# Optimization experiments

Hardware: AMD Instinct MI355X
Metric: run time of the kernel (lower is better)

## Reference

```python
import jax, jax.numpy as jnp
import numpy as np

T = 32          # n_node_types
EXTRA = 3       # input_dim = T + 3
D = 9           # perfect binary tree depth -> N = 2**D - 1 = 511 nodes/plan
N = 2 ** D - 1
EMB = 64
HID = 64
FC = 64
OUT = 8         # N_METRICS
NS = 5          # N_SAMPLES
P = 2560        # number of plans (P // NS = 512 groups)
B = 512


def setup_inputs() -> dict:
    key = jax.random.key(0)
    ks = jax.random.split(key, 8)

    def lin(k, o, i):
        return (jax.random.normal(k, (o, i), jnp.float32) / np.sqrt(i)).astype(jnp.float32)

    x0 = jax.random.normal(ks[0], (P, N, T + EXTRA), jnp.float32)
    x = jax.random.uniform(ks[1], (B, P // NS), jnp.float32)
    return {
        "x": x,
        "x0": x0,
        "W_emb": lin(ks[2], EMB, T), "b_emb": jnp.zeros((EMB,), jnp.float32),
        "W0": lin(ks[3], HID, EMB + EXTRA), "b0": jnp.zeros((HID,), jnp.float32),
        "W1": lin(ks[4], HID, EMB + EXTRA + 2 * HID), "b1": jnp.zeros((HID,), jnp.float32),
        "Wfc1": lin(ks[5], FC, HID), "bfc1": jnp.zeros((FC,), jnp.float32),
        "Wfc2": lin(ks[6], OUT, FC), "bfc2": jnp.zeros((OUT,), jnp.float32),
    }


def reference(x, x0, W_emb, b_emb, W0, b0, W1, b1, Wfc1, bfc1, Wfc2, bfc2):
    # --- enc_dnn: per-node embed + concat(extra, children hiddens) + Linear + ReLU ---
    # node_emb = emb(xi[:T]); node_input = [node_emb, xi[T:], h_children...]
    emb = jnp.einsum('pnt,et->pne', x0[..., :T], W_emb) + b_emb    # [P,N,EMB]
    feats = jnp.concatenate([emb, x0[..., T:]], axis=-1)           # [P,N,EMB+3]
    # heap layout: node i's children are 2i+1, 2i+2; level l occupies [2^l-1, 2^{l+1}-1)
    lo = 2 ** (D - 1) - 1
    h = jax.nn.relu(jnp.einsum('pnf,hf->pnh', feats[:, lo:], W0) + b0)  # leaves
    for l in range(D - 2, -1, -1):  # structural loop over tree levels (fixed, small)
        lo, n = 2 ** l - 1, 2 ** l
        f = feats[:, lo:lo + n]
        inp = jnp.concatenate([f, h[:, 0::2], h[:, 1::2]], axis=-1)  # [emb|extra|h_left|h_right]
        h = jax.nn.relu(jnp.einsum('pnf,hf->pnh', inp, W1) + b1)
    h0 = h[:, 0]                                                   # root hidden, [P,HID]
    # --- agg_weight ---
    mean_h = h0.reshape(-1, NS, HID).mean(axis=1)                  # [P/NS, HID]
    weighted = x @ mean_h                                          # [B, HID]
    hid = jax.nn.relu(weighted @ Wfc1.T + bfc1)
    return hid @ Wfc2.T + bfc2                                     # [B, OUT]
```

## Files before the change

### kernel.cpp

```cpp
#include <hip/hip_runtime.h>
#include <hip/hip_bf16.h>


typedef __attribute__((ext_vector_type(8))) short s8v;
typedef __attribute__((ext_vector_type(4))) float f4v;
typedef unsigned short u16;
typedef unsigned int   u32;

__device__ __forceinline__ u16 f2bf(float f) {
    return __builtin_bit_cast(u16, __float2bfloat16(f));
}
__device__ __forceinline__ f4v mfma16(s8v a, s8v b, f4v c) {
    return __builtin_amdgcn_mfma_f32_16x16x32_bf16(a, b, c, 0, 0, 0);
}
#define SWZ(r) ((((r) & 1) | (((r) >> 1) & 6)) << 3)

__device__ __forceinline__ u32 pk2(float a, float b) {
    return (u32)f2bf(fmaxf(a, 0.f)) | ((u32)f2bf(fmaxf(b, 0.f)) << 16);
}
__device__ __forceinline__ s8v pkfrag(f4v h0, f4v h1) {
    int4 d;
    d.x = (int)pk2(h0[0], h0[1]); d.y = (int)pk2(h0[2], h0[3]);
    d.z = (int)pk2(h1[0], h1[1]); d.w = (int)pk2(h1[2], h1[3]);
    return __builtin_bit_cast(s8v, d);
}
__device__ __forceinline__ s8v mkB0(float4 A, float4 B) {
    s8v r;
    r[0]=(short)f2bf(A.x); r[1]=(short)f2bf(A.y); r[2]=(short)f2bf(A.z); r[3]=(short)f2bf(A.w);
    r[4]=(short)f2bf(B.x); r[5]=(short)f2bf(B.y); r[6]=(short)f2bf(B.z); r[7]=(short)f2bf(B.w);
    return r;
}
__device__ __forceinline__ s8v mkB1(float4 T) {
    s8v r = (s8v){0,0,0,0,0,0,0,0};
    r[0]=(short)f2bf(T.y); r[1]=(short)f2bf(T.z); r[2]=(short)f2bf(T.w);
    return r;
}
__device__ __forceinline__ s8v xB0(const float* __restrict__ xr, int lq) {
    return mkB0(*(const float4*)(xr + lq * 8), *(const float4*)(xr + lq * 8 + 4));
}
__device__ __forceinline__ s8v xB1(const float* __restrict__ xr, int lq) {
    s8v r = (s8v){0,0,0,0,0,0,0,0};
    if (lq == 0) {
        float4 T = *(const float4*)(xr + 31);
        r[0]=(short)f2bf(T.y); r[1]=(short)f2bf(T.z); r[2]=(short)f2bf(T.w);
    }
    return r;
}
__device__ __forceinline__ s8v wread(const u16* w, int stride, int row, int ks, int lq) {
    return *(const s8v*)(w + row * stride + ks * 32 + lq * 8);
}
__device__ __forceinline__ f4v bias4(const float* __restrict__ b) {
    float4 t = *(const float4*)b; return (f4v){t.x, t.y, t.z, t.w};
}
__device__ __forceinline__ int sigp(int rho, int s, int h) {
    return 32*s + 4*h + ((rho & 12) << 1) + (rho & 3);
}

__global__ void prep_kernel(const float* __restrict__ W_emb, const float* __restrict__ b_emb,
                            const float* __restrict__ W0, const float* __restrict__ b0,
                            const float* __restrict__ W1, const float* __restrict__ b1,
                            u16* __restrict__ wt1, u16* __restrict__ wt0,
                            float* __restrict__ b1p, float* __restrict__ b0p)
{
    int idx = blockIdx.x * 256 + threadIdx.x;
    if (idx < 64 * 192) {
        int h = idx / 192, k = idx % 192;
        float v;
        if (k < 32) { v = 0.f; for (int e = 0; e < 64; e++) v = fmaf(W1[h*195+e], W_emb[e*32+k], v); }
        else if (k < 35)  v = W1[h*195 + 64 + (k - 32)];
        else if (k < 64)  v = 0.f;
        else              v = W1[h*195 + 67 + (k - 64)];
        wt1[h*192 + k] = f2bf(v);
    } else if (idx < 64*192 + 64*64) {
        int j = idx - 64*192; int h = j >> 6, k = j & 63;
        float v;
        if (k < 32)      { v = 0.f; for (int e = 0; e < 64; e++) v = fmaf(W0[h*67+e], W_emb[e*32+k], v); }
        else if (k < 35)   v = W0[h*67 + 64 + (k - 32)];
        else               v = 0.f;
        wt0[h*64 + k] = f2bf(v);
    } else if (idx < 64*192 + 64*64 + 64) {
        int h = idx - (64*192 + 64*64);
        float v = b1[h];
        for (int e = 0; e < 64; e++) v = fmaf(W1[h*195+e], b_emb[e], v);
        b1p[h] = v;
    } else if (idx < 64*192 + 64*64 + 128) {
        int h = idx - (64*192 + 64*64 + 64);
        float v = b0[h];
        for (int e = 0; e < 64; e++) v = fmaf(W0[h*67+e], b_emb[e], v);
        b0p[h] = v;
    }
}

__global__ __launch_bounds__(512, 2) void tree_all(
    const float* __restrict__ x0,
    const u16* __restrict__ wt1g, const u16* __restrict__ wt0g,
    const float* __restrict__ b1p, const float* __restrict__ b0p,
    float* __restrict__ h0out)
{
    __shared__ __align__(16) u16 wt1s[64 * 200];
    __shared__ __align__(16) u16 wt0s[64 * 40 + 64];
    __shared__ __align__(16) u16 buf6[4 * 64 * 64];

    const int tid = threadIdx.x;
    const int l   = tid & 63;
    const int w   = tid >> 6;
    const int lq  = l >> 4;
    const int rho = l & 15;
    const int pair = w >> 2;
    const int c    = w & 3;
    const int tA = blockIdx.x * 4 + 2 * pair;
    const int tB = tA + 1;
    const float* xbA = x0 + (size_t)tA * 511 * 35;
    const float* xbB = x0 + (size_t)tB * 511 * 35;

    const float* xq0A = xbA + (size_t)(255 + 64*c + 4*rho) * 35;
    const float* xq0B = xbB + (size_t)(255 + 64*c + 4*rho) * 35;
    float4 pAa = *(const float4*)(xq0A + lq*8);
    float4 pAb = *(const float4*)(xq0A + lq*8 + 4);
    float4 pAt = (lq == 0) ? *(const float4*)(xq0A + 31) : float4{0.f,0.f,0.f,0.f};
    float4 pBa = *(const float4*)(xq0B + lq*8);
    float4 pBb = *(const float4*)(xq0B + lq*8 + 4);
    float4 pBt = (lq == 0) ? *(const float4*)(xq0B + 31) : float4{0.f,0.f,0.f,0.f};

    {
        u32* d1 = (u32*)wt1s; const u32* s1 = (const u32*)wt1g;
        #pragma unroll
        for (int t = 0; t < 12; t++) {
            int i = t*512 + tid;
            int row = i / 96, kk = i - row*96;
            d1[row*100 + kk] = s1[row*96 + kk];
        }
        u32* d0 = (u32*)wt0s; const u32* s0 = (const u32*)wt0g;
        #pragma unroll
        for (int t = 0; t < 3; t++) {
            int i = t*512 + tid;
            if (i < 1280) { int row = i / 20, kk = i - row*20; d0[row*20 + kk] = s0[row*32 + kk]; }
        }
        if (tid < 32) ((u32*)(wt0s + 64*40))[tid] = 0;
    }
    __syncthreads();

    s8v TLA[4][2], TLB[4][2];
    {
        s8v WL[4][2]; f4v bL[4];
        #pragma unroll
        for (int i = 0; i < 4; i++) {
            int sg = sigp(rho, i >> 1, i & 1);
            WL[i][0] = wread(wt0s, 40, sg, 0, lq);
            WL[i][1] = wread(wt0s, 40, sg, 1, lq);
            bL[i] = bias4(b0p + 32*(i>>1) + 8*lq + 4*(i&1));
        }
        auto leafstep = [&](s8v xaA, s8v xtA, s8v xaB, s8v xtB, int q) {
            f4v aA[4], aB[4];
            #pragma unroll
            for (int i = 0; i < 4; i++) { aA[i] = bL[i]; aB[i] = bL[i]; }
            #pragma unroll
            for (int i = 0; i < 4; i++) {
                aA[i] = mfma16(WL[i][0], xaA, aA[i]);
                aA[i] = mfma16(WL[i][1], xtA, aA[i]);
                aB[i] = mfma16(WL[i][0], xaB, aB[i]);
                aB[i] = mfma16(WL[i][1], xtB, aB[i]);
            }
            TLA[q][0] = pkfrag(aA[0], aA[1]); TLA[q][1] = pkfrag(aA[2], aA[3]);
            TLB[q][0] = pkfrag(aB[0], aB[1]); TLB[q][1] = pkfrag(aB[2], aB[3]);
        };
        leafstep(mkB0(pAa, pAb), mkB1(pAt), mkB0(pBa, pBb), mkB1(pBt), 0);
        #pragma unroll
        for (int q = 1; q < 4; q++) {
            const float* xrA = xbA + (size_t)(255 + 64*c + 4*rho + q) * 35;
            const float* xrB = xbB + (size_t)(255 + 64*c + 4*rho + q) * 35;
            leafstep(xB0(xrA, lq), xB1(xrA, lq), xB0(xrB, lq), xB1(xrB, lq), q);
        }
    }

    s8v A7[4], B7[4];
    {
        f4v aAE[4], aAO[4], aBE[4], aBO[4];
        #pragma unroll
        for (int i = 0; i < 4; i++) {
            f4v b = bias4(b1p + 32*(i>>1) + 8*lq + 4*(i&1));
            aAE[i] = b; aAO[i] = b; aBE[i] = b; aBO[i] = b;
        }
        {
            const float* xrAE = xbA + (size_t)(127 + 32*c + 2*rho) * 35;
            const float* xrBE = xbB + (size_t)(127 + 32*c + 2*rho) * 35;
            s8v xAE0 = xB0(xrAE, lq),      xAE1 = xB1(xrAE, lq);
            s8v xAO0 = xB0(xrAE + 35, lq), xAO1 = xB1(xrAE + 35, lq);
            s8v xBE0 = xB0(xrBE, lq),      xBE1 = xB1(xrBE, lq);
            s8v xBO0 = xB0(xrBE + 35, lq), xBO1 = xB1(xrBE + 35, lq);
            #pragma unroll
            for (int i = 0; i < 4; i++) {
                int sg = sigp(rho, i >> 1, i & 1);
                s8v w0 = wread(wt1s, 200, sg, 0, lq);
                s8v w1 = wread(wt1s, 200, sg, 1, lq);
                aAE[i] = mfma16(w0, xAE0, aAE[i]); aAE[i] = mfma16(w1, xAE1, aAE[i]);
                aAO[i] = mfma16(w0, xAO0, aAO[i]); aAO[i] = mfma16(w1, xAO1, aAO[i]);
                aBE[i] = mfma16(w0, xBE0, aBE[i]); aBE[i] = mfma16(w1, xBE1, aBE[i]);
                aBO[i] = mfma16(w0, xBO0, aBO[i]); aBO[i] = mfma16(w1, xBO1, aBO[i]);
            }
        }
        #pragma unroll
        for (int i = 0; i < 4; i++) {
            int sg = sigp(rho, i >> 1, i & 1);
            s8v w2 = wread(wt1s, 200, sg, 2, lq);
            s8v w3 = wread(wt1s, 200, sg, 3, lq);
            s8v w4 = wread(wt1s, 200, sg, 4, lq);
            s8v w5 = wread(wt1s, 200, sg, 5, lq);
            aAE[i] = mfma16(w2, TLA[0][0], aAE[i]); aAE[i] = mfma16(w3, TLA[0][1], aAE[i]);
            aAE[i] = mfma16(w4, TLA[1][0], aAE[i]); aAE[i] = mfma16(w5, TLA[1][1], aAE[i]);
            aAO[i] = mfma16(w2, TLA[2][0], aAO[i]); aAO[i] = mfma16(w3, TLA[2][1], aAO[i]);
            aAO[i] = mfma16(w4, TLA[3][0], aAO[i]); aAO[i] = mfma16(w5, TLA[3][1], aAO[i]);
            aBE[i] = mfma16(w2, TLB[0][0], aBE[i]); aBE[i] = mfma16(w3, TLB[0][1], aBE[i]);
            aBE[i] = mfma16(w4, TLB[1][0], aBE[i]); aBE[i] = mfma16(w5, TLB[1][1], aBE[i]);
            aBO[i] = mfma16(w2, TLB[2][0], aBO[i]); aBO[i] = mfma16(w3, TLB[2][1], aBO[i]);
            aBO[i] = mfma16(w4, TLB[3][0], aBO[i]); aBO[i] = mfma16(w5, TLB[3][1], aBO[i]);
        }
        A7[0] = pkfrag(aAE[0], aAE[1]); A7[1] = pkfrag(aAE[2], aAE[3]);
        A7[2] = pkfrag(aAO[0], aAO[1]); A7[3] = pkfrag(aAO[2], aAO[3]);
        B7[0] = pkfrag(aBE[0], aBE[1]); B7[1] = pkfrag(aBE[2], aBE[3]);
        B7[2] = pkfrag(aBO[0], aBO[1]); B7[3] = pkfrag(aBO[2], aBO[3]);
    }

    {
        const float* xrA6 = xbA + (size_t)(63 + 16*c + rho) * 35;
        const float* xrB6 = xbB + (size_t)(63 + 16*c + rho) * 35;
        s8v xA0 = xB0(xrA6, lq), xA1 = xB1(xrA6, lq);
        s8v xBv0 = xB0(xrB6, lq), xBv1 = xB1(xrB6, lq);
        u16* slA = buf6 + (2*pair) * 4096;
        u16* slB = slA + 4096;
        int r6 = 16*c + rho;
        int sw6 = SWZ(r6);
        #pragma unroll
        for (int cc = 0; cc < 4; cc++) {
            int sg = 16*cc + rho;
            s8v w0 = wread(wt1s, 200, sg, 0, lq);
            s8v w1 = wread(wt1s, 200, sg, 1, lq);
            s8v w2 = wread(wt1s, 200, sg, 2, lq);
            s8v w3 = wread(wt1s, 200, sg, 3, lq);
            s8v w4 = wread(wt1s, 200, sg, 4, lq);
            s8v w5 = wread(wt1s, 200, sg, 5, lq);
            f4v bb = bias4(b1p + 16*cc + 4*lq);
            f4v aA = bb, aB = bb;
            aA = mfma16(w0, xA0, aA);  aA = mfma16(w1, xA1, aA);
            aA = mfma16(w2, A7[0], aA); aA = mfma16(w3, A7[1], aA);
            aA = mfma16(w4, A7[2], aA); aA = mfma16(w5, A7[3], aA);
            aB = mfma16(w0, xBv0, aB); aB = mfma16(w1, xBv1, aB);
            aB = mfma16(w2, B7[0], aB); aB = mfma16(w3, B7[1], aB);
            aB = mfma16(w4, B7[2], aB); aB = mfma16(w5, B7[3], aB);
            int col = (16*cc + 4*lq) ^ sw6;
            uint2 dA; dA.x = pk2(aA[0], aA[1]); dA.y = pk2(aA[2], aA[3]);
            uint2 dB; dB.x = pk2(aB[0], aB[1]); dB.y = pk2(aB[2], aB[3]);
            *(uint2*)(slA + (size_t)r6 * 64 + col) = dA;
            *(uint2*)(slB + (size_t)r6 * 64 + col) = dB;
        }
    }
    __syncthreads();

    const int  tt   = w & 3;
    const int  half = (w >= 4) ? 1 : 0;
    {
        const int tree = blockIdx.x * 4 + tt;
        u16* slice = buf6 + tt * 4096;
        const float* xb = x0 + (size_t)tree * 511 * 35;

        s8v ch5[2][2];
        #pragma unroll
        for (int pr = 0; pr < 2; pr++) {
            int row = 4*rho + 2*half + pr;
            int sw = SWZ(row);
            ch5[pr][0] = *(const s8v*)(slice + (size_t)row*64 + ((     8*lq) ^ sw));
            ch5[pr][1] = *(const s8v*)(slice + (size_t)row*64 + ((32 + 8*lq) ^ sw));
        }
        const float* xr5 = xb + (size_t)(31 + 2*rho + half) * 35;
        s8v x50 = xB0(xr5, lq), x51 = xB1(xr5, lq);
        f4v a5[4];
        #pragma unroll
        for (int i = 0; i < 4; i++) a5[i] = bias4(b1p + 32*(i>>1) + 8*lq + 4*(i&1));
        #pragma unroll
        for (int i = 0; i < 4; i++) {
            int sg = sigp(rho, i >> 1, i & 1);
            s8v w0 = wread(wt1s, 200, sg, 0, lq);
            s8v w1 = wread(wt1s, 200, sg, 1, lq);
            s8v w2 = wread(wt1s, 200, sg, 2, lq);
            s8v w3 = wread(wt1s, 200, sg, 3, lq);
            s8v w4 = wread(wt1s, 200, sg, 4, lq);
            s8v w5 = wread(wt1s, 200, sg, 5, lq);
            a5[i] = mfma16(w0, x50, a5[i]);      a5[i] = mfma16(w1, x51, a5[i]);
            a5[i] = mfma16(w2, ch5[0][0], a5[i]); a5[i] = mfma16(w3, ch5[0][1], a5[i]);
            a5[i] = mfma16(w4, ch5[1][0], a5[i]); a5[i] = mfma16(w5, ch5[1][1], a5[i]);
        }
        s8v L5X0 = pkfrag(a5[0], a5[1]), L5X1 = pkfrag(a5[2], a5[3]);

        __syncthreads();
        if (half == 1) {
            *(s8v*)(slice + 1024 + (size_t)l * 8) = L5X0;
            *(s8v*)(slice + 1536 + (size_t)l * 8) = L5X1;
        }
        __syncthreads();

        if (half == 0) {
            s8v L5E0 = L5X0, L5E1 = L5X1;
            s8v L5O0 = *(const s8v*)(slice + 1024 + (size_t)l * 8);
            s8v L5O1 = *(const s8v*)(slice + 1536 + (size_t)l * 8);

            {
                const float* xr4 = xb + (size_t)(15 + rho) * 35;
                s8v x40 = xB0(xr4, lq), x41 = xB1(xr4, lq);
                int sw4 = SWZ(rho);
                #pragma unroll
                for (int cc = 0; cc < 4; cc++) {
                    int sg = 16*cc + rho;
                    s8v w0 = wread(wt1s, 200, sg, 0, lq);
                    s8v w1 = wread(wt1s, 200, sg, 1, lq);
                    s8v w2 = wread(wt1s, 200, sg, 2, lq);
                    s8v w3 = wread(wt1s, 200, sg, 3, lq);
                    s8v w4 = wread(wt1s, 200, sg, 4, lq);
                    s8v w5 = wread(wt1s, 200, sg, 5, lq);
                    f4v a = bias4(b1p + 16*cc + 4*lq);
                    a = mfma16(w0, x40, a);  a = mfma16(w1, x41, a);
                    a = mfma16(w2, L5E0, a); a = mfma16(w3, L5E1, a);
                    a = mfma16(w4, L5O0, a); a = mfma16(w5, L5O1, a);
                    int col = (16*cc + 4*lq) ^ sw4;
                    uint2 d; d.x = pk2(a[0], a[1]); d.y = pk2(a[2], a[3]);
                    *(uint2*)(slice + (size_t)rho * 64 + col) = d;
                }
            }
            asm volatile("s_waitcnt lgkmcnt(0)" ::: "memory");

            u16* tb0 = slice + 32 * 64;
            u16* tb1 = slice;
            float bv[4];
            #pragma unroll
            for (int ct = 0; ct < 4; ct++) bv[ct] = b1p[ct*16 + rho];
            f4v acc[4];

            auto tlevel = [&](int lo, const u16* cb) {
                const float* xr = xb + (size_t)(lo + rho) * 35;
                s8v a0 = xB0(xr, lq), a1 = xB1(xr, lq);
                #pragma unroll
                for (int ct = 0; ct < 4; ct++) acc[ct] = (f4v){bv[ct], bv[ct], bv[ct], bv[ct]};
                #pragma unroll
                for (int ct = 0; ct < 4; ct++) {
                    acc[ct] = mfma16(a0, wread(wt1s, 200, ct*16 + rho, 0, lq), acc[ct]);
                    acc[ct] = mfma16(a1, wread(wt1s, 200, ct*16 + rho, 1, lq), acc[ct]);
                }
                #pragma unroll
                for (int ks = 0; ks < 4; ks++) {
                    int k0 = ks*32 + lq*8;
                    int rr = 2*rho + (k0 >> 6);
                    s8v ach = *(const s8v*)(cb + (size_t)rr*64 + ((k0 & 63) ^ SWZ(rr)));
                    #pragma unroll
                    for (int ct = 0; ct < 4; ct++)
                        acc[ct] = mfma16(ach, wread(wt1s, 200, ct*16 + rho, 2 + ks, lq), acc[ct]);
                }
            };
            auto tstore = [&](u16* buf) {
                #pragma unroll
                for (int r = 0; r < 4; r++) {
                    int ro = lq*4 + r; int sw = SWZ(ro);
                    #pragma unroll
                    for (int ct = 0; ct < 4; ct++)
                        buf[ro*64 + ((ct*16 + rho) ^ sw)] = f2bf(fmaxf(acc[ct][r], 0.f));
                }
                asm volatile("s_waitcnt lgkmcnt(0)" ::: "memory");
            };

            tlevel(7, slice);  tstore(tb0);
            tlevel(3, tb0);    tstore(tb1);
            tlevel(1, tb1);    tstore(tb0);
            tlevel(0, tb0);
            if (lq == 0) {
                #pragma unroll
                for (int ct = 0; ct < 4; ct++)
                    h0out[(size_t)tree*64 + ct*16 + rho] = fmaxf(acc[ct][0], 0.f);
            }
        }
    }
}

__global__ void mean_kernel(const float* __restrict__ h0, float* __restrict__ mh)
{
    int idx = blockIdx.x * blockDim.x + threadIdx.x;
    if (idx < 512 * 64) {
        int g = idx >> 6, h = idx & 63;
        float s = 0.f;
        #pragma unroll
        for (int q = 0; q < 5; q++) s += h0[(size_t)(g * 5 + q) * 64 + h];
        mh[idx] = s * 0.2f;
    }
}

__global__ __launch_bounds__(64) void head_kernel(const float* __restrict__ x,
                                                  const float* __restrict__ mh,
                                                  const float* __restrict__ Wfc1,
                                                  const float* __restrict__ bfc1,
                                                  const float* __restrict__ Wfc2,
                                                  const float* __restrict__ bfc2,
                                                  float* __restrict__ out)
{
    __shared__ float sw[64];
    __shared__ float sh[64];
    int b = blockIdx.x, h = threadIdx.x;

    float a0 = 0.f, a1 = 0.f, a2 = 0.f, a3 = 0.f;
    const float* xr = x + (size_t)b * 512;
    for (int g = 0; g < 512; g += 4) {
        a0 = fmaf(xr[g + 0], mh[(g + 0) * 64 + h], a0);
        a1 = fmaf(xr[g + 1], mh[(g + 1) * 64 + h], a1);
        a2 = fmaf(xr[g + 2], mh[(g + 2) * 64 + h], a2);
        a3 = fmaf(xr[g + 3], mh[(g + 3) * 64 + h], a3);
    }
    sw[h] = (a0 + a1) + (a2 + a3);
    __syncthreads();

    float acc = bfc1[h];
    #pragma unroll 8
    for (int k = 0; k < 64; k++) acc = fmaf(Wfc1[h * 64 + k], sw[k], acc);
    sh[h] = fmaxf(acc, 0.f);
    __syncthreads();

    if (h < 8) {
        float o = bfc2[h];
        #pragma unroll 8
        for (int f = 0; f < 64; f++) o = fmaf(Wfc2[h * 64 + f], sh[f], o);
        out[(size_t)b * 8 + h] = o;
    }
}

extern "C" void kernel_launch(void* const* d_in, const int* in_sizes, int n_in,
                              void* d_out, int out_size, void* d_ws, size_t ws_size,
                              hipStream_t stream)
{
    (void)in_sizes; (void)n_in; (void)out_size; (void)ws_size;
    const float* x     = (const float*)d_in[0];
    const float* x0    = (const float*)d_in[1];
    const float* W_emb = (const float*)d_in[2];
    const float* b_emb = (const float*)d_in[3];
    const float* W0    = (const float*)d_in[4];
    const float* b0    = (const float*)d_in[5];
    const float* W1    = (const float*)d_in[6];
    const float* b1    = (const float*)d_in[7];
    const float* Wfc1  = (const float*)d_in[8];
    const float* bfc1  = (const float*)d_in[9];
    const float* Wfc2  = (const float*)d_in[10];
    const float* bfc2  = (const float*)d_in[11];
    float* out = (float*)d_out;

    u16* wt1   = (u16*)d_ws;
    u16* wt0   = wt1 + 64 * 192;
    float* b1p = (float*)(wt0 + 64 * 64);
    float* b0p = b1p + 64;
    float* h0  = b0p + 64;
    float* mh  = h0 + 2560 * 64;

    prep_kernel<<<65, 256, 0, stream>>>(W_emb, b_emb, W0, b0, W1, b1, wt1, wt0, b1p, b0p);
    tree_all<<<640, 512, 0, stream>>>(x0, wt1, wt0, b1p, b0p, h0);
    mean_kernel<<<128, 256, 0, stream>>>(h0, mh);
    head_kernel<<<512, 64, 0, stream>>>(x, mh, Wfc1, bfc1, Wfc2, bfc2, out);
}
```

Before: 89.92 us.

## Split upper tree levels across both wave halves by output column tiles

Previously only half the waves (half==0) computed tree levels 4 down to 0 while the other half idled after level 5. Now both wave halves share that work, each computing two of the four 16-column output tiles, and they exchange level-5 results through shared memory. This shortens the serial tail per tree. The cost is block-wide __syncthreads between levels in place of the wave-local waitcnt, which adds synchronisation overhead.

```diff
diff --git a/kernel.cpp b/kernel.cpp
--- a/kernel.cpp
+++ b/kernel.cpp
@@ -257,12 +257,13 @@
     __syncthreads();
 
     const int  tt   = w & 3;
-    const int  half = (w >= 4) ? 1 : 0;
-    {
-        const int tree = blockIdx.x * 4 + tt;
-        u16* slice = buf6 + tt * 4096;
-        const float* xb = x0 + (size_t)tree * 511 * 35;
-
+    const int  half = w >> 2;
+    const int  tree = blockIdx.x * 4 + tt;
+    u16* slice = buf6 + tt * 4096;
+    const float* xb = x0 + (size_t)tree * 511 * 35;
+
+    s8v L5E0, L5E1, L5O0, L5O1;
+    {
         s8v ch5[2][2];
         #pragma unroll
         for (int pr = 0; pr < 2; pr++) {
@@ -292,89 +293,86 @@
         s8v L5X0 = pkfrag(a5[0], a5[1]), L5X1 = pkfrag(a5[2], a5[3]);
 
         __syncthreads();
-        if (half == 1) {
-            *(s8v*)(slice + 1024 + (size_t)l * 8) = L5X0;
-            *(s8v*)(slice + 1536 + (size_t)l * 8) = L5X1;
-        }
+        *(s8v*)(slice + 1024 + half*1024 + (size_t)l*8) = L5X0;
+        *(s8v*)(slice + 1536 + half*1024 + (size_t)l*8) = L5X1;
         __syncthreads();
-
-        if (half == 0) {
-            s8v L5E0 = L5X0, L5E1 = L5X1;
-            s8v L5O0 = *(const s8v*)(slice + 1024 + (size_t)l * 8);
-            s8v L5O1 = *(const s8v*)(slice + 1536 + (size_t)l * 8);
-
-            {
-                const float* xr4 = xb + (size_t)(15 + rho) * 35;
-                s8v x40 = xB0(xr4, lq), x41 = xB1(xr4, lq);
-                int sw4 = SWZ(rho);
-                #pragma unroll
-                for (int cc = 0; cc < 4; cc++) {
-                    int sg = 16*cc + rho;
-                    s8v w0 = wread(wt1s, 200, sg, 0, lq);
-                    s8v w1 = wread(wt1s, 200, sg, 1, lq);
-                    s8v w2 = wread(wt1s, 200, sg, 2, lq);
-                    s8v w3 = wread(wt1s, 200, sg, 3, lq);
-                    s8v w4 = wread(wt1s, 200, sg, 4, lq);
-                    s8v w5 = wread(wt1s, 200, sg, 5, lq);
-                    f4v a = bias4(b1p + 16*cc + 4*lq);
-                    a = mfma16(w0, x40, a);  a = mfma16(w1, x41, a);
-                    a = mfma16(w2, L5E0, a); a = mfma16(w3, L5E1, a);
-                    a = mfma16(w4, L5O0, a); a = mfma16(w5, L5O1, a);
-                    int col = (16*cc + 4*lq) ^ sw4;
-                    uint2 d; d.x = pk2(a[0], a[1]); d.y = pk2(a[2], a[3]);
-                    *(uint2*)(slice + (size_t)rho * 64 + col) = d;
-                }
-            }
-            asm volatile("s_waitcnt lgkmcnt(0)" ::: "memory");
-
-            u16* tb0 = slice + 32 * 64;
-            u16* tb1 = slice;
-            float bv[4];
+        L5E0 = *(const s8v*)(slice + 1024 + (size_t)l*8);
+        L5E1 = *(const s8v*)(slice + 1536 + (size_t)l*8);
+        L5O0 = *(const s8v*)(slice + 2048 + (size_t)l*8);
+        L5O1 = *(const s8v*)(slice + 2560 + (size_t)l*8);
+    }
+
+    const int cb0 = half * 2;
+
+    {
+        const float* xr4 = xb + (size_t)(15 + rho) * 35;
+        s8v x40 = xB0(xr4, lq), x41 = xB1(xr4, lq);
+        int sw4 = SWZ(rho);
+        #pragma unroll
+        for (int j = 0; j < 2; j++) {
+            int cc = cb0 + j;
+            int sg = 16*cc + rho;
+            s8v w0 = wread(wt1s, 200, sg, 0, lq);
+            s8v w1 = wread(wt1s, 200, sg, 1, lq);
+            s8v w2 = wread(wt1s, 200, sg, 2, lq);
+            s8v w3 = wread(wt1s, 200, sg, 3, lq);
+            s8v w4 = wread(wt1s, 200, sg, 4, lq);
+            s8v w5 = wread(wt1s, 200, sg, 5, lq);
+            f4v a = bias4(b1p + 16*cc + 4*lq);
+            a = mfma16(w0, x40, a);  a = mfma16(w1, x41, a);
+            a = mfma16(w2, L5E0, a); a = mfma16(w3, L5E1, a);
+            a = mfma16(w4, L5O0, a); a = mfma16(w5, L5O1, a);
+            int col = (16*cc + 4*lq) ^ sw4;
+            uint2 d; d.x = pk2(a[0], a[1]); d.y = pk2(a[2], a[3]);
+            *(uint2*)(slice + (size_t)rho * 64 + col) = d;
+        }
+    }
+    __syncthreads();
+
+    u16* tb0 = slice + 32 * 64;
+    u16* tb1 = slice;
+    float bv[2];
+    bv[0] = b1p[cb0*16 + rho];
+    bv[1] = b1p[(cb0+1)*16 + rho];
+    f4v acc[2];
+
+    auto tlevel = [&](int lo, const u16* cb) {
+        const float* xr = xb + (size_t)(lo + rho) * 35;
+        s8v a0 = xB0(xr, lq), a1 = xB1(xr, lq);
+        #pragma unroll
+        for (int j = 0; j < 2; j++) acc[j] = (f4v){bv[j], bv[j], bv[j], bv[j]};
+        #pragma unroll
+        for (int j = 0; j < 2; j++) {
+            acc[j] = mfma16(a0, wread(wt1s, 200, (cb0+j)*16 + rho, 0, lq), acc[j]);
+            acc[j] = mfma16(a1, wread(wt1s, 200, (cb0+j)*16 + rho, 1, lq), acc[j]);
+        }
+        #pragma unroll
+        for (int ks = 0; ks < 4; ks++) {
+            int k0 = ks*32 + lq*8;
+            int rr = 2*rho + (k0 >> 6);
+            s8v ach = *(const s8v*)(cb + (size_t)rr*64 + ((k0 & 63) ^ SWZ(rr)));
             #pragma unroll
-            for (int ct = 0; ct < 4; ct++) bv[ct] = b1p[ct*16 + rho];
-            f4v acc[4];
-
-            auto tlevel = [&](int lo, const u16* cb) {
-                const float* xr = xb + (size_t)(lo + rho) * 35;
-                s8v a0 = xB0(xr, lq), a1 = xB1(xr, lq);
-                #pragma unroll
-                for (int ct = 0; ct < 4; ct++) acc[ct] = (f4v){bv[ct], bv[ct], bv[ct], bv[ct]};
-                #pragma unroll
-                for (int ct = 0; ct < 4; ct++) {
-                    acc[ct] = mfma16(a0, wread(wt1s, 200, ct*16 + rho, 0, lq), acc[ct]);
-                    acc[ct] = mfma16(a1, wread(wt1s, 200, ct*16 + rho, 1, lq), acc[ct]);
-                }
-                #pragma unroll
-                for (int ks = 0; ks < 4; ks++) {
-                    int k0 = ks*32 + lq*8;
-                    int rr = 2*rho + (k0 >> 6);
-                    s8v ach = *(const s8v*)(cb + (size_t)rr*64 + ((k0 & 63) ^ SWZ(rr)));
-                    #pragma unroll
-                    for (int ct = 0; ct < 4; ct++)
-                        acc[ct] = mfma16(ach, wread(wt1s, 200, ct*16 + rho, 2 + ks, lq), acc[ct]);
-                }
-            };
-            auto tstore = [&](u16* buf) {
-                #pragma unroll
-                for (int r = 0; r < 4; r++) {
-                    int ro = lq*4 + r; int sw = SWZ(ro);
-                    #pragma unroll
-                    for (int ct = 0; ct < 4; ct++)
-                        buf[ro*64 + ((ct*16 + rho) ^ sw)] = f2bf(fmaxf(acc[ct][r], 0.f));
-                }
-                asm volatile("s_waitcnt lgkmcnt(0)" ::: "memory");
-            };
-
-            tlevel(7, slice);  tstore(tb0);
-            tlevel(3, tb0);    tstore(tb1);
-            tlevel(1, tb1);    tstore(tb0);
-            tlevel(0, tb0);
-            if (lq == 0) {
-                #pragma unroll
-                for (int ct = 0; ct < 4; ct++)
-                    h0out[(size_t)tree*64 + ct*16 + rho] = fmaxf(acc[ct][0], 0.f);
-            }
-        }
+            for (int j = 0; j < 2; j++)
+                acc[j] = mfma16(ach, wread(wt1s, 200, (cb0+j)*16 + rho, 2 + ks, lq), acc[j]);
+        }
+    };
+    auto tstore = [&](u16* buf) {
+        #pragma unroll
+        for (int r = 0; r < 4; r++) {
+            int ro = lq*4 + r; int sw = SWZ(ro);
+            #pragma unroll
+            for (int j = 0; j < 2; j++)
+                buf[ro*64 + (((cb0+j)*16 + rho) ^ sw)] = f2bf(fmaxf(acc[j][r], 0.f));
+        }
+    };
+
+    tlevel(7, slice);  tstore(tb0);  __syncthreads();
+    tlevel(3, tb0);    tstore(tb1);  __syncthreads();
+    tlevel(1, tb1);    tstore(tb0);  __syncthreads();
+    tlevel(0, tb0);
+    if (lq == 0) {
+        h0out[(size_t)tree*64 + cb0*16      + rho] = fmaxf(acc[0][0], 0.f);
+        h0out[(size_t)tree*64 + (cb0+1)*16  + rho] = fmaxf(acc[1][0], 0.f);
     }
 }
 
```

After: 93.49 us. +4.0%, slower.
